# Optimization experiments

Hardware: AMD Instinct MI355X
Metric: run time of the kernel (lower is better)

Reference implementation:

```python
import jax, jax.numpy as jnp
import numpy as np

B, T, HOR = 4096, 128, 24
EH, DH, A = 64, 64, 32


def setup_inputs() -> dict:
    key = jax.random.key(0)
    ks = jax.random.split(key, 21)
    g = lambda k, shape, s=0.1: (jax.random.normal(k, shape, jnp.float32) * s)
    return {
        "x": jax.random.normal(ks[0], (B, T, 1), jnp.float32),
        # encoder GRUCell (input_size=1)
        "W_ih_e": g(ks[1], (3 * EH, 1)), "W_hh_e": g(ks[2], (3 * EH, EH)),
        "b_ih_e": g(ks[3], (3 * EH,)), "b_hh_e": g(ks[4], (3 * EH,)),
        # encoder input attention
        "W_e": g(ks[5], (A, EH)), "U_e": g(ks[6], (1, A)),
        "b_e": jnp.zeros((1, A), jnp.float32), "v_e": g(ks[7], (A,)),
        # decoder init
        "W_init": g(ks[8], (DH, EH)), "b_init": g(ks[9], (DH,)),
        # decoder GRUCell (input_size=1)
        "W_ih_d": g(ks[10], (3 * DH, 1)), "W_hh_d": g(ks[11], (3 * DH, DH)),
        "b_ih_d": g(ks[12], (3 * DH,)), "b_hh_d": g(ks[13], (3 * DH,)),
        # temporal attention
        "W_d": g(ks[14], (A, DH)), "U_d": g(ks[15], (A, EH)), "v_d": g(ks[16], (A,)),
        # output head
        "W_out": g(ks[17], (1, DH + EH)), "b_out": g(ks[18], (1,)),
        "y0": jnp.zeros((1,), jnp.float32),
    }


def _gru_cell(x, h, W_ih, W_hh, b_ih, b_hh):
    # PyTorch GRUCell semantics
    gi = x @ W_ih.T + b_ih  # (B, 3H)
    gh = h @ W_hh.T + b_hh
    ir, iz, inn = jnp.split(gi, 3, axis=1)
    hr, hz, hn = jnp.split(gh, 3, axis=1)
    r = jax.nn.sigmoid(ir + hr)
    z = jax.nn.sigmoid(iz + hz)
    n = jnp.tanh(inn + r * hn)
    return (1.0 - z) * n + z * h


def reference(x, W_ih_e, W_hh_e, b_ih_e, b_hh_e, W_e, U_e, b_e, v_e,
              W_init, b_init, W_ih_d, W_hh_d, b_ih_d, b_hh_d,
              W_d, U_d, v_d, W_out, b_out, y0):
    bsz = x.shape[0]

    def enc_step(h, x_t):  # x_t: (B, 1)
        h_proj = h @ W_e.T  # (B, A)
        attn = jnp.tanh(h_proj[:, None, :] + x_t[:, :, None] * U_e[None] + b_e[None])  # (B,1,A)
        scores = jnp.sum(attn * v_e, axis=2)  # (B, 1)
        alpha = jax.nn.softmax(scores, axis=1)
        h_new = _gru_cell(alpha * x_t, h, W_ih_e, W_hh_e, b_ih_e, b_hh_e)
        return h_new, h_new

    h0 = jnp.zeros((bsz, EH), x.dtype)
    h_T, Hs = jax.lax.scan(enc_step, h0, jnp.swapaxes(x, 0, 1))  # Hs: (T,B,EH)
    H = jnp.swapaxes(Hs, 0, 1)  # (B, T, EH)

    d0 = h_T @ W_init.T + b_init  # (B, DH)
    H_proj = jnp.einsum('bte,ae->bta', H, U_d)  # hoisted: constant across decoder steps
    dec_in0 = jnp.broadcast_to(y0[None, :], (bsz, 1))

    def dec_step(carry, _):
        d, dec_in = carry
        d = _gru_cell(dec_in, d, W_ih_d, W_hh_d, b_ih_d, b_hh_d)
        d_proj = d @ W_d.T  # (B, A)
        attn = jnp.tanh(d_proj[:, None, :] + H_proj)  # (B, T, A)
        beta = jax.nn.softmax(jnp.sum(attn * v_d, axis=2), axis=1)  # (B, T)
        ctx = jnp.einsum('bt,bte->be', beta, H)  # (B, EH)
        out = jnp.concatenate([d, ctx], axis=1) @ W_out.T + b_out  # (B, 1)
        return (d, out), out[:, 0]

    (_, _), outs = jax.lax.scan(dec_step, (d0, dec_in0), None, length=HOR)
    return outs.T  # (B, horizon)
```

## Files before the change

kernel.cpp:

```cpp
#include <hip/hip_runtime.h>
#include <math.h>

#define BATCH 4096
#define T 128
#define HOR 24

#define LOG2E 1.44269504088896f
#define C2    2.88539008177793f

typedef _Float16 half2_t __attribute__((ext_vector_type(2)));
typedef _Float16 half8   __attribute__((ext_vector_type(8)));
typedef float f2  __attribute__((ext_vector_type(2)));
typedef float f4v __attribute__((ext_vector_type(4)));

__device__ __forceinline__ float fexp2(float x){ return __builtin_amdgcn_exp2f(x); }
__device__ __forceinline__ float frcp(float x){ return __builtin_amdgcn_rcpf(x); }
__device__ __forceinline__ float fsig(float x){ return frcp(1.0f + fexp2(-LOG2E*x)); }
__device__ __forceinline__ float ftanh(float x){ return fmaf(-2.0f, frcp(1.0f + fexp2(C2*x)), 1.0f); }
__device__ __forceinline__ half2_t bch(unsigned u){ return __builtin_bit_cast(half2_t,u); }
__device__ __forceinline__ unsigned pk2(float a,float b){ return __builtin_bit_cast(unsigned, __builtin_amdgcn_cvt_pkrtz(a,b)); }
__device__ __forceinline__ unsigned pk2rne(float a,float b){
  half2_t h; h.x = (_Float16)a; h.y = (_Float16)b;
  return __builtin_bit_cast(unsigned, h);
}
__device__ __forceinline__ float fdot2f(half2_t a, half2_t b, float c){
#if __has_builtin(__builtin_amdgcn_fdot2)
  return __builtin_amdgcn_fdot2(a,b,c,false);
#else
  return fmaf((float)a.x,(float)b.x, fmaf((float)a.y,(float)b.y,c));
#endif
}
__device__ __forceinline__ f2 pkfma(f2 a, f2 b, f2 c){ return __builtin_elementwise_fma(a,b,c); }

template <int CTRL, int RMASK>
__device__ __forceinline__ float dpp_add(float v) {
  int s = __builtin_amdgcn_update_dpp(0, __builtin_bit_cast(int, v), CTRL, RMASK, 0xf, true);
  return v + __builtin_bit_cast(float, s);
}
__device__ __forceinline__ float wavesum_dpp(float v) {
  v = dpp_add<0x111, 0xf>(v);
  v = dpp_add<0x112, 0xf>(v);
  v = dpp_add<0x114, 0xf>(v);
  v = dpp_add<0x118, 0xf>(v);
  v = dpp_add<0x142, 0xa>(v);
  v = dpp_add<0x143, 0xc>(v);
  return v;
}
__device__ __forceinline__ float rdl63(float v){
  return __builtin_bit_cast(float, __builtin_amdgcn_readlane(__builtin_bit_cast(int, v), 63));
}

#define WG_BARRIER_LDS() do {                                   \
    asm volatile("s_waitcnt lgkmcnt(0)" ::: "memory");          \
    __builtin_amdgcn_s_barrier();                               \
  } while (0)

__device__ __forceinline__ void gru_mv(const _Float16* hrow,
    const unsigned* wr_r, const unsigned* wr_z, const unsigned* wr_n,
    float& ar0, float& ar1, float& az0, float& az1, float& an0, float& an1)
{
  const uint4* hq = (const uint4*)hrow;
  #pragma unroll
  for (int q = 0; q < 8; ++q) {
    uint4 hv = hq[q];
    ar0 = fdot2f(bch(hv.x), bch(wr_r[4*q+0]), ar0);
    az0 = fdot2f(bch(hv.x), bch(wr_z[4*q+0]), az0);
    an0 = fdot2f(bch(hv.x), bch(wr_n[4*q+0]), an0);
    ar1 = fdot2f(bch(hv.y), bch(wr_r[4*q+1]), ar1);
    az1 = fdot2f(bch(hv.y), bch(wr_z[4*q+1]), az1);
    an1 = fdot2f(bch(hv.y), bch(wr_n[4*q+1]), an1);
    ar0 = fdot2f(bch(hv.z), bch(wr_r[4*q+2]), ar0);
    az0 = fdot2f(bch(hv.z), bch(wr_z[4*q+2]), az0);
    an0 = fdot2f(bch(hv.z), bch(wr_n[4*q+2]), an0);
    ar1 = fdot2f(bch(hv.w), bch(wr_r[4*q+3]), ar1);
    az1 = fdot2f(bch(hv.w), bch(wr_z[4*q+3]), az1);
    an1 = fdot2f(bch(hv.w), bch(wr_n[4*q+3]), an1);
  }
}

__device__ __forceinline__ float proj_dot(const _Float16* base, const unsigned* udr)
{
  float acc = 0.f;
  const uint4* hb = (const uint4*)base;
  #pragma unroll
  for (int q = 0; q < 4; ++q) {
    uint4 hv = hb[q];
    acc = fdot2f(bch(hv.x), bch(udr[4*q+0]), acc);
    acc = fdot2f(bch(hv.y), bch(udr[4*q+1]), acc);
    acc = fdot2f(bch(hv.z), bch(udr[4*q+2]), acc);
    acc = fdot2f(bch(hv.w), bch(udr[4*q+3]), acc);
  }
  return acc;
}

__device__ __forceinline__ half8 cvt8(f4v a, f4v b){
  half8 h;
  h[0]=(_Float16)a.x; h[1]=(_Float16)a.y; h[2]=(_Float16)a.z; h[3]=(_Float16)a.w;
  h[4]=(_Float16)b.x; h[5]=(_Float16)b.y; h[6]=(_Float16)b.z; h[7]=(_Float16)b.w;
  return h;
}

__global__ __launch_bounds__(256, 1)
void darnn_enc(const float* __restrict__ x,
               const float* __restrict__ W_ih_e, const float* __restrict__ W_hh_e,
               const float* __restrict__ b_ih_e, const float* __restrict__ b_hh_e,
               const float* __restrict__ U_d, const float* __restrict__ W_out,
               unsigned* __restrict__ hpG, float* __restrict__ hTG)
{
  const int tid = threadIdx.x;
  const int w = tid >> 6;
  const int l = tid & 63;
  const int c = l & 15;
  const int q = l >> 4;
  const int e0 = blockIdx.x * 16;
  const int m0 = 16*w + 4*q;

  __shared__ __align__(16) _Float16 He[2][16*72];
  __shared__ __align__(16) unsigned xw[16*65];

  for (int idx = tid; idx < 16*64; idx += 256) {
    int e = idx >> 6, j = idx & 63;
    f2 g = ((const f2*)(x + (size_t)(e0+e)*T))[j];
    xw[e*65 + j] = pk2(g.x, g.y);
  }
  for (int idx = tid; idx < 576; idx += 256) ((unsigned*)He[0])[idx] = 0;

  half8 Ar[2], Az[2], An[2];
  #pragma unroll
  for (int kap = 0; kap < 2; ++kap) {
    const f4v* pr = (const f4v*)(W_hh_e + (size_t)(16*w + c)*64       + 32*kap + 8*q);
    const f4v* pz = (const f4v*)(W_hh_e + (size_t)(64 + 16*w + c)*64  + 32*kap + 8*q);
    const f4v* pn = (const f4v*)(W_hh_e + (size_t)(128 + 16*w + c)*64 + 32*kap + 8*q);
    Ar[kap] = cvt8(pr[0], pr[1]);
    Az[kap] = cvt8(pz[0], pz[1]);
    An[kap] = cvt8(pn[0], pn[1]);
  }
  half8 AX[2] = {{0,0,0,0,0,0,0,0},{0,0,0,0,0,0,0,0}};
  if (w < 2) {
    #pragma unroll
    for (int kap = 0; kap < 2; ++kap) {
      const f4v* p = (const f4v*)(U_d + (size_t)(16*w + c)*64 + 32*kap + 8*q);
      AX[kap] = cvt8(p[0] * C2, p[1] * C2);
    }
  } else if (w == 2 && c == 0) {
    #pragma unroll
    for (int kap = 0; kap < 2; ++kap) {
      const f4v* p = (const f4v*)(W_out + 64 + 32*kap + 8*q);
      AX[kap] = cvt8(p[0], p[1]);
    }
  }
  f4v wih0 = *(const f4v*)(W_ih_e + m0);
  f4v wih1 = *(const f4v*)(W_ih_e + 64 + m0);
  f4v wih2 = *(const f4v*)(W_ih_e + 128 + m0);
  f4v bb0  = *(const f4v*)(b_ih_e + m0)      + *(const f4v*)(b_hh_e + m0);
  f4v bb1  = *(const f4v*)(b_ih_e + 64 + m0) + *(const f4v*)(b_hh_e + 64 + m0);
  f4v bi2  = *(const f4v*)(b_ih_e + 128 + m0);
  f4v bh2  = *(const f4v*)(b_hh_e + 128 + m0);
  f4v hreg = {0,0,0,0};
  const f4v z4 = {0,0,0,0};
  unsigned* hpB = hpG + (size_t)(e0 + c) * 2176;

  __syncthreads();

  #pragma unroll 1
  for (int t = 0; t < T; ++t) {
    const _Float16* Hc = He[t & 1];
    half8 B0 = __builtin_bit_cast(half8, *(const uint4*)(Hc + c*72 + 8*q));
    half8 B1 = __builtin_bit_cast(half8, *(const uint4*)(Hc + c*72 + 32 + 8*q));
    if (t > 0) {
      if (w < 2) {
        f4v cu = __builtin_amdgcn_mfma_f32_16x16x32_f16(AX[0], B0, z4, 0,0,0);
        cu     = __builtin_amdgcn_mfma_f32_16x16x32_f16(AX[1], B1, cu, 0,0,0);
        unsigned* hpE = hpB + (t-1)*17 + 8*w;
        float x0 = fexp2(fminf(cu[0], 15.5f));
        float x1 = fexp2(fminf(cu[1], 15.5f));
        float x2 = fexp2(fminf(cu[2], 15.5f));
        float x3 = fexp2(fminf(cu[3], 15.5f));
        hpE[2*q]   = pk2rne(x0, x1);
        hpE[2*q+1] = pk2rne(x2, x3);
      } else if (w == 2) {
        f4v cw = __builtin_amdgcn_mfma_f32_16x16x32_f16(AX[0], B0, z4, 0,0,0);
        cw     = __builtin_amdgcn_mfma_f32_16x16x32_f16(AX[1], B1, cw, 0,0,0);
        if (q == 0) ((float*)(hpB + (t-1)*17))[16] = cw[0];
      }
    }
    f4v gr = __builtin_amdgcn_mfma_f32_16x16x32_f16(Ar[0], B0, z4, 0,0,0);
    gr     = __builtin_amdgcn_mfma_f32_16x16x32_f16(Ar[1], B1, gr, 0,0,0);
    f4v gz = __builtin_amdgcn_mfma_f32_16x16x32_f16(Az[0], B0, z4, 0,0,0);
    gz     = __builtin_amdgcn_mfma_f32_16x16x32_f16(Az[1], B1, gz, 0,0,0);
    f4v gn = __builtin_amdgcn_mfma_f32_16x16x32_f16(An[0], B0, z4, 0,0,0);
    gn     = __builtin_amdgcn_mfma_f32_16x16x32_f16(An[1], B1, gn, 0,0,0);
    float xc = (float)((const _Float16*)xw)[c*130 + t];
    f4v hn;
    #pragma unroll
    for (int i = 0; i < 4; ++i) {
      float r  = fsig(fmaf(xc, wih0[i], bb0[i]) + gr[i]);
      float zf = fsig(fmaf(xc, wih1[i], bb1[i]) + gz[i]);
      float n  = ftanh(fmaf(xc, wih2[i], bi2[i]) + r*(gn[i] + bh2[i]));
      float h  = fmaf(zf, hreg[i] - n, n);
      hreg[i] = h;
      hn[i] = h;
    }
    uint2 wv; wv.x = pk2(hn[0], hn[1]); wv.y = pk2(hn[2], hn[3]);
    *(uint2*)(He[(t+1)&1] + c*72 + m0) = wv;
    WG_BARRIER_LDS();
  }
  {
    const _Float16* Hc = He[0];
    half8 B0 = __builtin_bit_cast(half8, *(const uint4*)(Hc + c*72 + 8*q));
    half8 B1 = __builtin_bit_cast(half8, *(const uint4*)(Hc + c*72 + 32 + 8*q));
    if (w < 2) {
      f4v cu = __builtin_amdgcn_mfma_f32_16x16x32_f16(AX[0], B0, z4, 0,0,0);
      cu     = __builtin_amdgcn_mfma_f32_16x16x32_f16(AX[1], B1, cu, 0,0,0);
      unsigned* hpE = hpB + 127*17 + 8*w;
      float x0 = fexp2(fminf(cu[0], 15.5f));
      float x1 = fexp2(fminf(cu[1], 15.5f));
      float x2 = fexp2(fminf(cu[2], 15.5f));
      float x3 = fexp2(fminf(cu[3], 15.5f));
      hpE[2*q]   = pk2rne(x0, x1);
      hpE[2*q+1] = pk2rne(x2, x3);
    } else if (w == 2) {
      f4v cw = __builtin_amdgcn_mfma_f32_16x16x32_f16(AX[0], B0, z4, 0,0,0);
      cw     = __builtin_amdgcn_mfma_f32_16x16x32_f16(AX[1], B1, cw, 0,0,0);
      if (q == 0) ((float*)(hpB + 127*17))[16] = cw[0];
    }
  }
  #pragma unroll
  for (int i = 0; i < 4; ++i)
    hTG[(size_t)(e0 + c)*64 + m0 + i] = hreg[i];
}

__global__ __launch_bounds__(128, 2)
void darnn_dec(const float* __restrict__ W_init, const float* __restrict__ b_init,
               const float* __restrict__ W_ih_d, const float* __restrict__ W_hh_d,
               const float* __restrict__ b_ih_d, const float* __restrict__ b_hh_d,
               const float* __restrict__ W_d, const float* __restrict__ v_d,
               const float* __restrict__ W_out, const float* __restrict__ b_out,
               const float* __restrict__ y0,
               const unsigned* __restrict__ hpG, const float* __restrict__ hTG,
               float* __restrict__ out)
{
  const int tid = threadIdx.x;
  const int wid = tid >> 6;
  const int l   = tid & 63;
  const int b   = 2*blockIdx.x + wid;
  const int a    = l & 31;
  const int half = l >> 5;

  __shared__ __align__(16) unsigned char smem[18496];
  unsigned char* wbp = smem + wid*9248;
  unsigned* sh_hp   = (unsigned*)wbp;
  _Float16* sh_ring = (_Float16*)(wbp + 8704);
  float*    sh_hT   = (float*)(wbp + 8864);
  float*    sh_dp   = (float*)(wbp + 9120);

  {
    const uint4* src = (const uint4*)(hpG + (size_t)b * 2176);
    #pragma unroll
    for (int it = 0; it < 8; ++it)
      ((uint4*)sh_hp)[it*64 + l] = src[it*64 + l];
    const unsigned* s2 = hpG + (size_t)b*2176 + 2048;
    sh_hp[2048 + l] = s2[l];
    sh_hp[2112 + l] = s2[64 + l];
  }
  sh_hT[l] = hTG[(size_t)b*64 + l];

  unsigned wr_r[32], wr_z[32], wr_n[32];
  {
    const f4v* wp = (const f4v*)W_hh_d;
    #pragma unroll
    for (int k = 0; k < 16; ++k) {
      f4v vr = wp[l*16 + k];
      f4v vz = wp[(64 + l)*16 + k];
      f4v vn = wp[(128 + l)*16 + k];
      wr_r[2*k] = pk2(vr.x, vr.y); wr_r[2*k+1] = pk2(vr.z, vr.w);
      wr_z[2*k] = pk2(vz.x, vz.y); wr_z[2*k+1] = pk2(vz.z, vz.w);
      wr_n[2*k] = pk2(vn.x, vn.y); wr_n[2*k+1] = pk2(vn.z, vn.w);
    }
  }
  float wih0 = W_ih_d[l], wih1 = W_ih_d[64+l], wih2 = W_ih_d[128+l];
  float bb0  = b_ih_d[l] + b_hh_d[l];
  float bb1  = b_ih_d[64+l] + b_hh_d[64+l];
  float bih2 = b_ih_d[128+l], bhh2 = b_hh_d[128+l];
  unsigned udr[16];
  {
    const f2* up = (const f2*)(W_d + a*64 + half*32);
    #pragma unroll
    for (int k = 0; k < 16; ++k) { f2 f = up[k]; udr[k] = pk2(f.x, f.y); }
  }
  float dprev;
  {
    const f4v* wi = (const f4v*)(W_init + l*64);
    const f4v* hb = (const f4v*)sh_hT;
    f2 a0={0,0}, a1={0,0};
    #pragma unroll
    for (int k = 0; k < 16; ++k) {
      f4v wv = wi[k]; f4v hv = hb[k];
      a0 = pkfma(wv.xy, hv.xy, a0);
      a1 = pkfma(wv.zw, hv.zw, a1);
    }
    dprev = b_init[l] + (a0.x + a0.y) + (a1.x + a1.y);
  }
  float wout1 = W_out[l];
  float hw0 = __builtin_bit_cast(float, sh_hp[l*17 + 16]);
  float hw1 = __builtin_bit_cast(float, sh_hp[(64 + l)*17 + 16]);
  float oprev = y0[0];
  float bo = b_out[0];
  float c1;
  {
    float sv = v_d[a];
    sv += __shfl_xor(sv, 16); sv += __shfl_xor(sv, 8);
    sv += __shfl_xor(sv, 4);  sv += __shfl_xor(sv, 2); sv += __shfl_xor(sv, 1);
    c1 = LOG2E * sv;
  }
  sh_ring[l] = (_Float16)dprev;

  const unsigned* hpr0 = sh_hp + l*17;
  const unsigned* hpr1 = sh_hp + (64 + l)*17;

  #pragma unroll 1
  for (int s = 0; s < HOR; ++s) {
    float ar0=0,ar1=0,az0=0,az1=0,an0=0,an1=0;
    gru_mv(sh_ring, wr_r, wr_z, wr_n, ar0,ar1,az0,az1,an0,an1);
    float r = fsig(fmaf(oprev, wih0, bb0) + ar0 + ar1);
    float z = fsig(fmaf(oprev, wih1, bb1) + az0 + az1);
    float n = ftanh(fmaf(oprev, wih2, bih2) + r * (an0 + an1 + bhh2));
    float dnew = fmaf(z, dprev - n, n);
    dprev = dnew;
    sh_ring[l] = (_Float16)dnew;
    {
      float acc = proj_dot(sh_ring + half*32, udr);
      acc += __shfl_xor(acc, 32);
      if (l < 32) sh_dp[l] = fexp2(C2 * acc);
    }
    float rs0 = 0.f, rs1 = 0.f;
    #pragma unroll
    for (int j2 = 0; j2 < 8; ++j2) {
      f4v ed = *(const f4v*)&sh_dp[4*j2];
      half2_t ha0 = bch(hpr0[2*j2]), hb0 = bch(hpr0[2*j2+1]);
      half2_t ha1 = bch(hpr1[2*j2]), hb1 = bch(hpr1[2*j2+1]);
      float v0 = v_d[4*j2], v1 = v_d[4*j2+1], v2 = v_d[4*j2+2], v3 = v_d[4*j2+3];
      rs0 = fmaf(v0, frcp(fmaf(ed.x, (float)ha0.x, 1.0f)), rs0);
      rs0 = fmaf(v1, frcp(fmaf(ed.y, (float)ha0.y, 1.0f)), rs0);
      rs0 = fmaf(v2, frcp(fmaf(ed.z, (float)hb0.x, 1.0f)), rs0);
      rs0 = fmaf(v3, frcp(fmaf(ed.w, (float)hb0.y, 1.0f)), rs0);
      rs1 = fmaf(v0, frcp(fmaf(ed.x, (float)ha1.x, 1.0f)), rs1);
      rs1 = fmaf(v1, frcp(fmaf(ed.y, (float)ha1.y, 1.0f)), rs1);
      rs1 = fmaf(v2, frcp(fmaf(ed.z, (float)hb1.x, 1.0f)), rs1);
      rs1 = fmaf(v3, frcp(fmaf(ed.w, (float)hb1.y, 1.0f)), rs1);
    }
    float e0 = fexp2(fmaf(-C2, rs0, c1));
    float e1 = fexp2(fmaf(-C2, rs1, c1));
    float P0 = rdl63(wavesum_dpp(e0 + e1));
    float P1 = rdl63(wavesum_dpp(fmaf(e0, hw0, e1 * hw1)));
    float P2 = rdl63(wavesum_dpp(wout1 * dnew));
    float o = fmaf(P1, frcp(P0), P2 + bo);
    if (l == 0) out[(size_t)b * HOR + s] = o;
    oprev = o;
  }
}

extern "C" void kernel_launch(void* const* d_in, const int* in_sizes, int n_in,
                              void* d_out, int out_size, void* d_ws, size_t ws_size,
                              hipStream_t stream) {
  const float* x      = (const float*)d_in[0];
  const float* W_ih_e = (const float*)d_in[1];
  const float* W_hh_e = (const float*)d_in[2];
  const float* b_ih_e = (const float*)d_in[3];
  const float* b_hh_e = (const float*)d_in[4];
  const float* W_init = (const float*)d_in[9];
  const float* b_init = (const float*)d_in[10];
  const float* W_ih_d = (const float*)d_in[11];
  const float* W_hh_d = (const float*)d_in[12];
  const float* b_ih_d = (const float*)d_in[13];
  const float* b_hh_d = (const float*)d_in[14];
  const float* W_d    = (const float*)d_in[15];
  const float* U_d    = (const float*)d_in[16];
  const float* v_d    = (const float*)d_in[17];
  const float* W_out  = (const float*)d_in[18];
  const float* b_out  = (const float*)d_in[19];
  const float* y0     = (const float*)d_in[20];
  float* outp = (float*)d_out;

  unsigned* hpG = (unsigned*)d_ws;
  float*    hTG = (float*)((char*)d_ws + (size_t)BATCH * 2176 * 4);

  darnn_enc<<<BATCH/16, 256, 0, stream>>>(x, W_ih_e, W_hh_e, b_ih_e, b_hh_e,
      U_d, W_out, hpG, hTG);
  darnn_dec<<<BATCH/2, 128, 0, stream>>>(W_init, b_init, W_ih_d, W_hh_d,
      b_ih_d, b_hh_d, W_d, v_d, W_out, b_out, y0, hpG, hTG, outp);
}
```

Measured before the change: 268.9 us.

## Stage encoder attention outputs in LDS chunks; interleave two batch rows per decoder wave

The encoder now writes its per-step exp-projected hidden values into a double-buffered LDS staging area and flushes each 16-step chunk to global memory with coalesced stores, instead of scattered per-lane global stores every step. The decoder processes two batch elements per wave, sharing register-resident weights and interleaving the two independent recurrences to hide latency. Grid size halves for the decoder. This raises LDS use and register pressure in both kernels, which may lower occupancy.

```diff
diff --git a/kernel.cpp b/kernel.cpp
--- a/kernel.cpp
+++ b/kernel.cpp
@@ -117,6 +117,7 @@
 
   __shared__ __align__(16) _Float16 He[2][16*72];
   __shared__ __align__(16) unsigned xw[16*65];
+  __shared__ __align__(16) unsigned ehC[2][16*273];
 
   for (int idx = tid; idx < 16*64; idx += 256) {
     int e = idx >> 6, j = idx & 63;
@@ -158,30 +159,41 @@
   f4v bh2  = *(const f4v*)(b_hh_e + 128 + m0);
   f4v hreg = {0,0,0,0};
   const f4v z4 = {0,0,0,0};
-  unsigned* hpB = hpG + (size_t)(e0 + c) * 2176;
 
   __syncthreads();
 
   #pragma unroll 1
   for (int t = 0; t < T; ++t) {
+    if ((t & 15) == 1 && t > 16) {
+      int cidx = (t - 17) >> 4;
+      const unsigned* sbuf = ehC[cidx & 1];
+      int t0 = cidx << 4;
+      #pragma unroll
+      for (int it = 0; it < 17; ++it) {
+        int idx = tid + it*256;
+        int e = idx / 272;
+        int o = idx - e*272;
+        hpG[(size_t)(e0+e)*2176 + t0*17 + o] = sbuf[e*273 + o];
+      }
+    }
     const _Float16* Hc = He[t & 1];
     half8 B0 = __builtin_bit_cast(half8, *(const uint4*)(Hc + c*72 + 8*q));
     half8 B1 = __builtin_bit_cast(half8, *(const uint4*)(Hc + c*72 + 32 + 8*q));
     if (t > 0) {
+      unsigned* eb = ehC[((t-1) >> 4) & 1] + c*273 + ((t-1) & 15)*17;
       if (w < 2) {
         f4v cu = __builtin_amdgcn_mfma_f32_16x16x32_f16(AX[0], B0, z4, 0,0,0);
         cu     = __builtin_amdgcn_mfma_f32_16x16x32_f16(AX[1], B1, cu, 0,0,0);
-        unsigned* hpE = hpB + (t-1)*17 + 8*w;
         float x0 = fexp2(fminf(cu[0], 15.5f));
         float x1 = fexp2(fminf(cu[1], 15.5f));
         float x2 = fexp2(fminf(cu[2], 15.5f));
         float x3 = fexp2(fminf(cu[3], 15.5f));
-        hpE[2*q]   = pk2rne(x0, x1);
-        hpE[2*q+1] = pk2rne(x2, x3);
+        eb[8*w + 2*q]   = pk2rne(x0, x1);
+        eb[8*w + 2*q+1] = pk2rne(x2, x3);
       } else if (w == 2) {
         f4v cw = __builtin_amdgcn_mfma_f32_16x16x32_f16(AX[0], B0, z4, 0,0,0);
         cw     = __builtin_amdgcn_mfma_f32_16x16x32_f16(AX[1], B1, cw, 0,0,0);
-        if (q == 0) ((float*)(hpB + (t-1)*17))[16] = cw[0];
+        if (q == 0) ((float*)eb)[16] = cw[0];
       }
     }
     f4v gr = __builtin_amdgcn_mfma_f32_16x16x32_f16(Ar[0], B0, z4, 0,0,0);
@@ -209,20 +221,31 @@
     const _Float16* Hc = He[0];
     half8 B0 = __builtin_bit_cast(half8, *(const uint4*)(Hc + c*72 + 8*q));
     half8 B1 = __builtin_bit_cast(half8, *(const uint4*)(Hc + c*72 + 32 + 8*q));
+    unsigned* eb = ehC[1] + c*273 + 15*17;
     if (w < 2) {
       f4v cu = __builtin_amdgcn_mfma_f32_16x16x32_f16(AX[0], B0, z4, 0,0,0);
       cu     = __builtin_amdgcn_mfma_f32_16x16x32_f16(AX[1], B1, cu, 0,0,0);
-      unsigned* hpE = hpB + 127*17 + 8*w;
       float x0 = fexp2(fminf(cu[0], 15.5f));
       float x1 = fexp2(fminf(cu[1], 15.5f));
       float x2 = fexp2(fminf(cu[2], 15.5f));
       float x3 = fexp2(fminf(cu[3], 15.5f));
-      hpE[2*q]   = pk2rne(x0, x1);
-      hpE[2*q+1] = pk2rne(x2, x3);
+      eb[8*w + 2*q]   = pk2rne(x0, x1);
+      eb[8*w + 2*q+1] = pk2rne(x2, x3);
     } else if (w == 2) {
       f4v cw = __builtin_amdgcn_mfma_f32_16x16x32_f16(AX[0], B0, z4, 0,0,0);
       cw     = __builtin_amdgcn_mfma_f32_16x16x32_f16(AX[1], B1, cw, 0,0,0);
-      if (q == 0) ((float*)(hpB + 127*17))[16] = cw[0];
+      if (q == 0) ((float*)eb)[16] = cw[0];
+    }
+  }
+  WG_BARRIER_LDS();
+  {
+    const unsigned* sbuf = ehC[1];
+    #pragma unroll
+    for (int it = 0; it < 17; ++it) {
+      int idx = tid + it*256;
+      int e = idx / 272;
+      int o = idx - e*272;
+      hpG[(size_t)(e0+e)*2176 + 112*17 + o] = sbuf[e*273 + o];
     }
   }
   #pragma unroll
@@ -243,27 +266,37 @@
   const int tid = threadIdx.x;
   const int wid = tid >> 6;
   const int l   = tid & 63;
-  const int b   = 2*blockIdx.x + wid;
+  const int bA  = 4*blockIdx.x + 2*wid;
+  const int bB  = bA + 1;
   const int a    = l & 31;
   const int half = l >> 5;
 
-  __shared__ __align__(16) unsigned char smem[18496];
-  unsigned char* wbp = smem + wid*9248;
-  unsigned* sh_hp   = (unsigned*)wbp;
-  _Float16* sh_ring = (_Float16*)(wbp + 8704);
-  float*    sh_hT   = (float*)(wbp + 8864);
-  float*    sh_dp   = (float*)(wbp + 9120);
-
-  {
-    const uint4* src = (const uint4*)(hpG + (size_t)b * 2176);
-    #pragma unroll
-    for (int it = 0; it < 8; ++it)
-      ((uint4*)sh_hp)[it*64 + l] = src[it*64 + l];
-    const unsigned* s2 = hpG + (size_t)b*2176 + 2048;
-    sh_hp[2048 + l] = s2[l];
-    sh_hp[2112 + l] = s2[64 + l];
-  }
-  sh_hT[l] = hTG[(size_t)b*64 + l];
+  __shared__ __align__(16) unsigned char smem[36928];
+  unsigned char* wbp = smem + wid*18464;
+  unsigned* hpA   = (unsigned*)wbp;
+  unsigned* hpB   = (unsigned*)(wbp + 8704);
+  _Float16* ringA = (_Float16*)(wbp + 17408);
+  _Float16* ringB = (_Float16*)(wbp + 17536);
+  float*    dpA   = (float*)(wbp + 17664);
+  float*    dpB   = (float*)(wbp + 17792);
+  float*    hTA   = (float*)(wbp + 17920);
+  float*    hTB   = (float*)(wbp + 18176);
+
+  {
+    const uint4* sA = (const uint4*)(hpG + (size_t)bA * 2176);
+    const uint4* sB = (const uint4*)(hpG + (size_t)bB * 2176);
+    #pragma unroll
+    for (int it = 0; it < 8; ++it) {
+      ((uint4*)hpA)[it*64 + l] = sA[it*64 + l];
+      ((uint4*)hpB)[it*64 + l] = sB[it*64 + l];
+    }
+    const unsigned* rA = hpG + (size_t)bA*2176 + 2048;
+    const unsigned* rB = hpG + (size_t)bB*2176 + 2048;
+    hpA[2048 + l] = rA[l];      hpA[2112 + l] = rA[64 + l];
+    hpB[2048 + l] = rB[l];      hpB[2112 + l] = rB[64 + l];
+  }
+  hTA[l] = hTG[(size_t)bA*64 + l];
+  hTB[l] = hTG[(size_t)bB*64 + l];
 
   unsigned wr_r[32], wr_z[32], wr_n[32];
   {
@@ -288,23 +321,31 @@
     #pragma unroll
     for (int k = 0; k < 16; ++k) { f2 f = up[k]; udr[k] = pk2(f.x, f.y); }
   }
-  float dprev;
+  float dprevA, dprevB;
   {
     const f4v* wi = (const f4v*)(W_init + l*64);
-    const f4v* hb = (const f4v*)sh_hT;
-    f2 a0={0,0}, a1={0,0};
+    const f4v* ga = (const f4v*)hTA;
+    const f4v* gb = (const f4v*)hTB;
+    f2 aa0={0,0}, aa1={0,0}, ba0={0,0}, ba1={0,0};
     #pragma unroll
     for (int k = 0; k < 16; ++k) {
-      f4v wv = wi[k]; f4v hv = hb[k];
-      a0 = pkfma(wv.xy, hv.xy, a0);
-      a1 = pkfma(wv.zw, hv.zw, a1);
-    }
-    dprev = b_init[l] + (a0.x + a0.y) + (a1.x + a1.y);
+      f4v wv = wi[k];
+      f4v va = ga[k], vb = gb[k];
+      aa0 = pkfma(wv.xy, va.xy, aa0);
+      aa1 = pkfma(wv.zw, va.zw, aa1);
+      ba0 = pkfma(wv.xy, vb.xy, ba0);
+      ba1 = pkfma(wv.zw, vb.zw, ba1);
+    }
+    float bi = b_init[l];
+    dprevA = bi + (aa0.x + aa0.y) + (aa1.x + aa1.y);
+    dprevB = bi + (ba0.x + ba0.y) + (ba1.x + ba1.y);
   }
   float wout1 = W_out[l];
-  float hw0 = __builtin_bit_cast(float, sh_hp[l*17 + 16]);
-  float hw1 = __builtin_bit_cast(float, sh_hp[(64 + l)*17 + 16]);
-  float oprev = y0[0];
+  float hw0A = __builtin_bit_cast(float, hpA[l*17 + 16]);
+  float hw1A = __builtin_bit_cast(float, hpA[(64 + l)*17 + 16]);
+  float hw0B = __builtin_bit_cast(float, hpB[l*17 + 16]);
+  float hw1B = __builtin_bit_cast(float, hpB[(64 + l)*17 + 16]);
+  float oprevA = y0[0], oprevB = y0[0];
   float bo = b_out[0];
   float c1;
   {
@@ -313,50 +354,85 @@
     sv += __shfl_xor(sv, 4);  sv += __shfl_xor(sv, 2); sv += __shfl_xor(sv, 1);
     c1 = LOG2E * sv;
   }
-  sh_ring[l] = (_Float16)dprev;
-
-  const unsigned* hpr0 = sh_hp + l*17;
-  const unsigned* hpr1 = sh_hp + (64 + l)*17;
+  ringA[l] = (_Float16)dprevA;
+  ringB[l] = (_Float16)dprevB;
+
+  const unsigned* hprA0 = hpA + l*17;
+  const unsigned* hprA1 = hpA + (64 + l)*17;
+  const unsigned* hprB0 = hpB + l*17;
+  const unsigned* hprB1 = hpB + (64 + l)*17;
 
   #pragma unroll 1
   for (int s = 0; s < HOR; ++s) {
-    float ar0=0,ar1=0,az0=0,az1=0,an0=0,an1=0;
-    gru_mv(sh_ring, wr_r, wr_z, wr_n, ar0,ar1,az0,az1,an0,an1);
-    float r = fsig(fmaf(oprev, wih0, bb0) + ar0 + ar1);
-    float z = fsig(fmaf(oprev, wih1, bb1) + az0 + az1);
-    float n = ftanh(fmaf(oprev, wih2, bih2) + r * (an0 + an1 + bhh2));
-    float dnew = fmaf(z, dprev - n, n);
-    dprev = dnew;
-    sh_ring[l] = (_Float16)dnew;
+    float ar0A=0,ar1A=0,az0A=0,az1A=0,an0A=0,an1A=0;
+    float ar0B=0,ar1B=0,az0B=0,az1B=0,an0B=0,an1B=0;
+    gru_mv(ringA, wr_r, wr_z, wr_n, ar0A,ar1A,az0A,az1A,an0A,an1A);
+    gru_mv(ringB, wr_r, wr_z, wr_n, ar0B,ar1B,az0B,az1B,an0B,an1B);
+    float rA = fsig(fmaf(oprevA, wih0, bb0) + ar0A + ar1A);
+    float zA = fsig(fmaf(oprevA, wih1, bb1) + az0A + az1A);
+    float nA = ftanh(fmaf(oprevA, wih2, bih2) + rA * (an0A + an1A + bhh2));
+    float dnewA = fmaf(zA, dprevA - nA, nA);
+    float rB = fsig(fmaf(oprevB, wih0, bb0) + ar0B + ar1B);
+    float zB = fsig(fmaf(oprevB, wih1, bb1) + az0B + az1B);
+    float nB = ftanh(fmaf(oprevB, wih2, bih2) + rB * (an0B + an1B + bhh2));
+    float dnewB = fmaf(zB, dprevB - nB, nB);
+    dprevA = dnewA; dprevB = dnewB;
+    ringA[l] = (_Float16)dnewA;
+    ringB[l] = (_Float16)dnewB;
     {
-      float acc = proj_dot(sh_ring + half*32, udr);
-      acc += __shfl_xor(acc, 32);
-      if (l < 32) sh_dp[l] = fexp2(C2 * acc);
-    }
-    float rs0 = 0.f, rs1 = 0.f;
+      float accA = proj_dot(ringA + half*32, udr);
+      float accB = proj_dot(ringB + half*32, udr);
+      accA += __shfl_xor(accA, 32);
+      accB += __shfl_xor(accB, 32);
+      if (l < 32) {
+        dpA[l] = fexp2(C2 * accA);
+        dpB[l] = fexp2(C2 * accB);
+      }
+    }
+    float rs0A = 0.f, rs1A = 0.f, rs0B = 0.f, rs1B = 0.f;
     #pragma unroll
     for (int j2 = 0; j2 < 8; ++j2) {
-      f4v ed = *(const f4v*)&sh_dp[4*j2];
-      half2_t ha0 = bch(hpr0[2*j2]), hb0 = bch(hpr0[2*j2+1]);
-      half2_t ha1 = bch(hpr1[2*j2]), hb1 = bch(hpr1[2*j2+1]);
+      f4v edA = *(const f4v*)&dpA[4*j2];
+      f4v edB = *(const f4v*)&dpB[4*j2];
+      half2_t haA0 = bch(hprA0[2*j2]), hbA0 = bch(hprA0[2*j2+1]);
+      half2_t haA1 = bch(hprA1[2*j2]), hbA1 = bch(hprA1[2*j2+1]);
+      half2_t haB0 = bch(hprB0[2*j2]), hbB0 = bch(hprB0[2*j2+1]);
+      half2_t haB1 = bch(hprB1[2*j2]), hbB1 = bch(hprB1[2*j2+1]);
       float v0 = v_d[4*j2], v1 = v_d[4*j2+1], v2 = v_d[4*j2+2], v3 = v_d[4*j2+3];
-      rs0 = fmaf(v0, frcp(fmaf(ed.x, (float)ha0.x, 1.0f)), rs0);
-      rs0 = fmaf(v1, frcp(fmaf(ed.y, (float)ha0.y, 1.0f)), rs0);
-      rs0 = fmaf(v2, frcp(fmaf(ed.z, (float)hb0.x, 1.0f)), rs0);
-      rs0 = fmaf(v3, frcp(fmaf(ed.w, (float)hb0.y, 1.0f)), rs0);
-      rs1 = fmaf(v0, frcp(fmaf(ed.x, (float)ha1.x, 1.0f)), rs1);
-      rs1 = fmaf(v1, frcp(fmaf(ed.y, (float)ha1.y, 1.0f)), rs1);
-      rs1 = fmaf(v2, frcp(fmaf(ed.z, (float)hb1.x, 1.0f)), rs1);
-      rs1 = fmaf(v3, frcp(fmaf(ed.w, (float)hb1.y, 1.0f)), rs1);
-    }
-    float e0 = fexp2(fmaf(-C2, rs0, c1));
-    float e1 = fexp2(fmaf(-C2, rs1, c1));
-    float P0 = rdl63(wavesum_dpp(e0 + e1));
-    float P1 = rdl63(wavesum_dpp(fmaf(e0, hw0, e1 * hw1)));
-    float P2 = rdl63(wavesum_dpp(wout1 * dnew));
-    float o = fmaf(P1, frcp(P0), P2 + bo);
-    if (l == 0) out[(size_t)b * HOR + s] = o;
-    oprev = o;
+      rs0A = fmaf(v0, frcp(fmaf(edA.x, (float)haA0.x, 1.0f)), rs0A);
+      rs0B = fmaf(v0, frcp(fmaf(edB.x, (float)haB0.x, 1.0f)), rs0B);
+      rs0A = fmaf(v1, frcp(fmaf(edA.y, (float)haA0.y, 1.0f)), rs0A);
+      rs0B = fmaf(v1, frcp(fmaf(edB.y, (float)haB0.y, 1.0f)), rs0B);
+      rs0A = fmaf(v2, frcp(fmaf(edA.z, (float)hbA0.x, 1.0f)), rs0A);
+      rs0B = fmaf(v2, frcp(fmaf(edB.z, (float)hbB0.x, 1.0f)), rs0B);
+      rs0A = fmaf(v3, frcp(fmaf(edA.w, (float)hbA0.y, 1.0f)), rs0A);
+      rs0B = fmaf(v3, frcp(fmaf(edB.w, (float)hbB0.y, 1.0f)), rs0B);
+      rs1A = fmaf(v0, frcp(fmaf(edA.x, (float)haA1.x, 1.0f)), rs1A);
+      rs1B = fmaf(v0, frcp(fmaf(edB.x, (float)haB1.x, 1.0f)), rs1B);
+      rs1A = fmaf(v1, frcp(fmaf(edA.y, (float)haA1.y, 1.0f)), rs1A);
+      rs1B = fmaf(v1, frcp(fmaf(edB.y, (float)haB1.y, 1.0f)), rs1B);
+      rs1A = fmaf(v2, frcp(fmaf(edA.z, (float)hbA1.x, 1.0f)), rs1A);
+      rs1B = fmaf(v2, frcp(fmaf(edB.z, (float)hbB1.x, 1.0f)), rs1B);
+      rs1A = fmaf(v3, frcp(fmaf(edA.w, (float)hbA1.y, 1.0f)), rs1A);
+      rs1B = fmaf(v3, frcp(fmaf(edB.w, (float)hbB1.y, 1.0f)), rs1B);
+    }
+    float e0A = fexp2(fmaf(-C2, rs0A, c1));
+    float e1A = fexp2(fmaf(-C2, rs1A, c1));
+    float e0B = fexp2(fmaf(-C2, rs0B, c1));
+    float e1B = fexp2(fmaf(-C2, rs1B, c1));
+    float P0A = rdl63(wavesum_dpp(e0A + e1A));
+    float P1A = rdl63(wavesum_dpp(fmaf(e0A, hw0A, e1A * hw1A)));
+    float P2A = rdl63(wavesum_dpp(wout1 * dnewA));
+    float P0B = rdl63(wavesum_dpp(e0B + e1B));
+    float P1B = rdl63(wavesum_dpp(fmaf(e0B, hw0B, e1B * hw1B)));
+    float P2B = rdl63(wavesum_dpp(wout1 * dnewB));
+    float oA = fmaf(P1A, frcp(P0A), P2A + bo);
+    float oB = fmaf(P1B, frcp(P0B), P2B + bo);
+    if (l == 0) {
+      out[(size_t)bA * HOR + s] = oA;
+      out[(size_t)bB * HOR + s] = oB;
+    }
+    oprevA = oA; oprevB = oB;
   }
 }
 
@@ -387,6 +463,6 @@
 
   darnn_enc<<<BATCH/16, 256, 0, stream>>>(x, W_ih_e, W_hh_e, b_ih_e, b_hh_e,
       U_d, W_out, hpG, hTG);
-  darnn_dec<<<BATCH/2, 128, 0, stream>>>(W_init, b_init, W_ih_d, W_hh_d,
+  darnn_dec<<<BATCH/4, 128, 0, stream>>>(W_init, b_init, W_ih_d, W_hh_d,
       b_ih_d, b_hh_d, W_d, v_d, W_out, b_out, y0, hpG, hTG, outp);
 }
```

Measured after the change: 272.1 us. About the same (+1.2%).
